# Kernel tuning notes

Measured on AMD Instinct MI355X. Metric: run time of the kernel, lower is better.

Reference implementation:

```python
import jax, jax.numpy as jnp
import numpy as np

B, GRID, WIDTH, NBLOCKS = 128, 32, 100, 50  # num_layers=100 -> 50 two-GEMM residual blocks


def _forward(inputs, W0, Wa, Wb, b1, b2, b3, b4, mult, Wout, bout):
    Bb, G = inputs.shape[0], inputs.shape[1]
    T = G // 2
    even = jnp.arange(0, G, 2)
    odd = even + 1
    idx = (even - 1) % G  # [(i-1) % G for even i]

    def patch(i1, i2):
        # gather axis1 then axis2 -> (B, T, T, 3, 3) flattened to (B*T*T, 9)
        return inputs[:, i1][:, :, i2].reshape(-1, 9)

    # order: right, left, up, down, center (matches tf.concat order)
    flat = jnp.concatenate([patch(odd, even), patch(idx, even), patch(even, odd),
                            patch(even, idx), patch(even, even)], axis=-1)  # (B*T*T, 45)

    x = jax.nn.relu(flat @ W0)  # (B*T*T, 100)

    def block(x, p):
        wa, wb, bb1, bb2, bb3, bb4, m = p
        x1 = (x + bb1) @ wa
        x1 = 2.0 * x1 + bb2          # x1 + bias_2 + x1
        x1 = jax.nn.relu(x1)
        x1 = 2.0 * x1 + bb3          # x1 + bias_3 + x1
        x1 = (x1 @ wb) * m
        x = jax.nn.relu(x + x1 + bb4)
        return x, None

    x, _ = jax.lax.scan(block, x, (Wa, Wb, b1, b2, b3, b4, mult))

    x = (x @ Wout + bout).reshape(Bb, T, T, 4)

    jp1 = (jnp.arange(T) + 1) % T
    jm1 = (jnp.arange(T) - 1) % T
    x0, x1c, x2, x3 = x[..., 0], x[..., 1], x[..., 2], x[..., 3]
    right_c = x0 / (x1c[:, jp1] + x0)
    left_c = x1c / (x1c + x0[:, jm1])
    up_c = x2 / (x2 + x3[:, :, jp1])
    down_c = x3 / (x2[:, :, jm1] + x3)

    # corner contributions from the original fine-grid stencils
    oo = inputs[:, odd][:, :, odd]    # odd-odd fine points (ru corner)
    oi = inputs[:, odd][:, :, idx]    # rd corner
    io = inputs[:, idx][:, :, odd]    # lu corner
    ii = inputs[:, idx][:, :, idx]    # ld corner
    ru = -(oo[..., 0, 0] + oo[..., 1, 0] * right_c + oo[..., 0, 1] * up_c) / oo[..., 1, 1]
    rd = -(oi[..., 0, 2] + oi[..., 1, 2] * right_c + oi[..., 0, 1] * down_c) / oi[..., 1, 1]
    lu = -(io[..., 2, 0] + io[..., 1, 0] * left_c + io[..., 2, 1] * up_c) / io[..., 1, 1]
    ld = -(ii[..., 2, 2] + ii[..., 1, 2] * left_c + ii[..., 2, 1] * down_c) / ii[..., 1, 1]

    ones = jnp.ones_like(down_c)
    first_row = jnp.stack([ld, left_c, lu], axis=-1)
    second_row = jnp.stack([down_c, ones, up_c], axis=-1)
    third_row = jnp.stack([rd, right_c, ru], axis=-1)
    out = jnp.stack([first_row, second_row, third_row], axis=0)  # (3, B, T, T, 3)
    return jnp.transpose(out, (1, 2, 3, 0, 4))  # (B, T, T, 3, 3)


def setup_inputs() -> dict:
    key = jax.random.key(0)
    ks = jax.random.split(key, 6)
    # positive stencil entries keep the corner divisions well-conditioned
    inputs = jax.random.uniform(ks[0], (B, GRID, GRID, 3, 3), jnp.float32) + 0.5
    W0 = jax.random.normal(ks[1], (45, WIDTH), jnp.float32) * np.float32(np.sqrt(2.0 / 45))
    Wa = jax.random.normal(ks[2], (NBLOCKS, WIDTH, WIDTH), jnp.float32) * np.float32(np.sqrt(2.0 / WIDTH))
    # original inits linear_{i+1} to zeros; small random keeps the baseline non-degenerate
    Wb = jax.random.normal(ks[3], (NBLOCKS, WIDTH, WIDTH), jnp.float32) * np.float32(0.01)
    b1 = jnp.zeros((NBLOCKS,), jnp.float32)
    b2 = jnp.zeros((NBLOCKS,), jnp.float32)
    b3 = jnp.zeros((NBLOCKS,), jnp.float32)
    b4 = jnp.zeros((NBLOCKS,), jnp.float32)
    mult = jnp.ones((NBLOCKS,), jnp.float32)
    Wout = jax.random.normal(ks[4], (WIDTH, 4), jnp.float32) * np.float32(0.05)
    bout = jnp.ones((4,), jnp.float32)  # keeps contribution denominators ~2 (stable)
    return {"inputs": inputs, "W0": W0, "Wa": Wa, "Wb": Wb, "b1": b1, "b2": b2,
            "b3": b3, "b4": b4, "mult": mult, "Wout": Wout, "bout": bout}


def reference(inputs, W0, Wa, Wb, b1, b2, b3, b4, mult, Wout, bout):
    return _forward(inputs, W0, Wa, Wb, b1, b2, b3, b4, mult, Wout, bout)
```

## Files before the change

kernel.cpp:

```cpp
#include <hip/hip_runtime.h>
#include <cstddef>

typedef _Float16 f16x8 __attribute__((ext_vector_type(8)));
typedef float f32x4 __attribute__((ext_vector_type(4)));

constexpr int BATCH = 128;
constexpr int T     = 16;
constexpr int ROWS  = BATCH * T * T;
constexpr int WID   = 100;
constexpr int NB    = 50;
constexpr int KP    = 128;
constexpr int NP    = 128;
constexpr int RPW   = 64;
constexpr int WCH   = 16384;

__global__ __launch_bounds__(256) void prep_kernel(
    const float* __restrict__ Wa, const float* __restrict__ Wb,
    _Float16* __restrict__ whi, _Float16* __restrict__ wlo,
    float* __restrict__ csA) {
  const int bid = blockIdx.x;
  const int bk = bid >> 1, m = bid & 1;
  const float* src = (m ? Wb : Wa) + (size_t)bk * (WID * WID);
  _Float16* dh = whi + (size_t)bid * WCH;
  _Float16* dl = wlo + (size_t)bid * WCH;
  for (int e = threadIdx.x; e < WCH; e += 256) {
    const int i   = e & 7;
    const int L   = (e >> 3) & 63;
    const int tau = (e >> 9) & 7;
    const int kap = e >> 12;
    const int k   = 32 * kap + (L >> 4) * 8 + i;
    const int col = 16 * tau + (L & 15);
    const float v = (k < WID && col < WID) ? src[k * WID + col] : 0.0f;
    const _Float16 hi = (_Float16)v;
    dh[e] = hi;
    dl[e] = (_Float16)(v - (float)hi);
  }
  if (!m) {
    for (int col = threadIdx.x; col < NP; col += 256) {
      float s = 0.0f;
      if (col < WID) {
        for (int k = 0; k < WID; ++k) s += src[k * WID + col];
      }
      csA[bk * NP + col] = s;
    }
  }
}

__global__ __launch_bounds__(256) void first_layer_kernel(
    const float* __restrict__ inp, const float* __restrict__ W0,
    float* __restrict__ x0) {
  __shared__ float w0s[45 * WID];
  for (int i = threadIdx.x; i < 45 * WID; i += 256) w0s[i] = W0[i];
  __syncthreads();

  const int rq  = threadIdx.x >> 2;
  const int cq  = threadIdx.x & 3;
  const int row = blockIdx.x * 64 + rq;
  const int b   = row >> 8;
  const int t1  = (row >> 4) & 15;
  const int t2  = row & 15;
  const int g1  = 2 * t1, g2 = 2 * t2;
  const int g1m = (g1 + 31) & 31, g2m = (g2 + 31) & 31;
  const float* base = inp + (size_t)b * (32 * 32 * 9);
  const float* p0 = base + ((g1 + 1) * 32 + g2) * 9;
  const float* p1 = base + (g1m * 32 + g2) * 9;
  const float* p2 = base + (g1 * 32 + (g2 + 1)) * 9;
  const float* p3 = base + (g1 * 32 + g2m) * 9;
  const float* p4 = base + (g1 * 32 + g2) * 9;

  float f[45];
#pragma unroll
  for (int qq = 0; qq < 9; ++qq) {
    f[qq]      = p0[qq];
    f[9 + qq]  = p1[qq];
    f[18 + qq] = p2[qq];
    f[27 + qq] = p3[qq];
    f[36 + qq] = p4[qq];
  }

  float acc[25];
#pragma unroll
  for (int j = 0; j < 25; ++j) acc[j] = 0.0f;
  const int j0 = cq * 25;
#pragma unroll
  for (int k = 0; k < 45; ++k) {
    const float fv = f[k];
#pragma unroll
    for (int j = 0; j < 25; ++j) acc[j] += fv * w0s[k * WID + j0 + j];
  }
  float* orow = x0 + (size_t)row * WID + j0;
#pragma unroll
  for (int j = 0; j < 25; ++j) orow[j] = fmaxf(acc[j], 0.0f);
}

__global__ __launch_bounds__(256, 2) void chain_kernel(
    float* __restrict__ x0,
    const _Float16* __restrict__ whi, const _Float16* __restrict__ wlo,
    const float* __restrict__ csA,
    const float* __restrict__ B1, const float* __restrict__ B2,
    const float* __restrict__ B3, const float* __restrict__ B4,
    const float* __restrict__ M) {
  __shared__ __align__(16) _Float16 xhs[RPW * KP];
  __shared__ __align__(16) _Float16 xls[RPW * KP];

  const int tid  = threadIdx.x;
  const int lane = tid & 63;
  const int uw   = __builtin_amdgcn_readfirstlane(tid >> 6);
  const int q    = lane >> 4;
  const int fr   = lane & 15;
  const int rbase = blockIdx.x * RPW;

  for (int i = tid; i < RPW * KP; i += 256) {
    const int row = i >> 7, k = i & 127;
    const float v = (k < WID) ? x0[(size_t)(rbase + row) * WID + k] : 0.0f;
    const _Float16 hi = (_Float16)v;
    const int a = row * KP + (k ^ ((row & 7) << 3));
    xhs[a] = hi;
    xls[a] = (_Float16)(v - (float)hi);
  }

  int colc[2];
#pragma unroll
  for (int c = 0; c < 2; ++c) colc[c] = 16 * (2 * uw + c) + fr;
  float xres[4][2][4];
#pragma unroll
  for (int rt = 0; rt < 4; ++rt)
#pragma unroll
    for (int c = 0; c < 2; ++c)
#pragma unroll
      for (int rg = 0; rg < 4; ++rg) {
        const int row = 16 * rt + 4 * q + rg;
        xres[rt][c][rg] = (colc[c] < WID)
            ? x0[(size_t)(rbase + row) * WID + colc[c]] : 0.0f;
      }
  __syncthreads();

  f32x4 acc[4][2];
  auto zero_acc = [&]() {
#pragma unroll
    for (int rt = 0; rt < 4; ++rt)
#pragma unroll
      for (int c = 0; c < 2; ++c) acc[rt][c] = (f32x4){0.f, 0.f, 0.f, 0.f};
  };

  auto kloop = [&](const _Float16* __restrict__ gh,
                   const _Float16* __restrict__ gl) {
    f16x8 bh[4][2], bl[4][2];
#pragma unroll
    for (int kap = 0; kap < 4; ++kap)
#pragma unroll
      for (int c = 0; c < 2; ++c) {
        const int off = (kap * 8 + 2 * uw + c) * 512 + lane * 8;
        bh[kap][c] = *(const f16x8*)&gh[off];
        bl[kap][c] = *(const f16x8*)&gl[off];
      }
#pragma unroll
    for (int kap = 0; kap < 4; ++kap) {
      f16x8 ah[4], al[4];
#pragma unroll
      for (int rt = 0; rt < 4; ++rt) {
        const int row = 16 * rt + fr;
        const int off = row * KP + ((32 * kap + 8 * q) ^ ((fr & 7) << 3));
        ah[rt] = *(const f16x8*)&xhs[off];
        al[rt] = *(const f16x8*)&xls[off];
      }
#pragma unroll
      for (int rt = 0; rt < 4; ++rt)
#pragma unroll
        for (int c = 0; c < 2; ++c) {
          acc[rt][c] = __builtin_amdgcn_mfma_f32_16x16x32_f16(
              ah[rt], bh[kap][c], acc[rt][c], 0, 0, 0);
          acc[rt][c] = __builtin_amdgcn_mfma_f32_16x16x32_f16(
              ah[rt], bl[kap][c], acc[rt][c], 0, 0, 0);
          acc[rt][c] = __builtin_amdgcn_mfma_f32_16x16x32_f16(
              al[rt], bh[kap][c], acc[rt][c], 0, 0, 0);
        }
    }
  };

  for (int bk = 0; bk < NB; ++bk) {
    zero_acc();
    kloop(whi + (size_t)(bk * 2) * WCH, wlo + (size_t)(bk * 2) * WCH);
    __syncthreads();
    {
      const float b1 = B1[bk], b2 = B2[bk], b3 = B3[bk];
      const float csv[2] = {csA[bk * NP + colc[0]], csA[bk * NP + colc[1]]};
#pragma unroll
      for (int rt = 0; rt < 4; ++rt)
#pragma unroll
        for (int c = 0; c < 2; ++c)
#pragma unroll
          for (int rg = 0; rg < 4; ++rg) {
            const int row = 16 * rt + 4 * q + rg;
            const float t = 2.0f * (acc[rt][c][rg] + b1 * csv[c]) + b2;
            const float v = 2.0f * fmaxf(t, 0.0f) + b3;
            const _Float16 hi = (_Float16)v;
            const int a = row * KP + (colc[c] ^ ((row & 7) << 3));
            xhs[a] = hi;
            xls[a] = (_Float16)(v - (float)hi);
          }
    }
    __syncthreads();

    zero_acc();
    kloop(whi + (size_t)(bk * 2 + 1) * WCH, wlo + (size_t)(bk * 2 + 1) * WCH);
    __syncthreads();
    {
      const float b4v = B4[bk], mm = M[bk];
#pragma unroll
      for (int rt = 0; rt < 4; ++rt)
#pragma unroll
        for (int c = 0; c < 2; ++c)
#pragma unroll
          for (int rg = 0; rg < 4; ++rg) {
            const int row = 16 * rt + 4 * q + rg;
            const float xn = fmaxf(xres[rt][c][rg] + acc[rt][c][rg] * mm + b4v, 0.0f);
            xres[rt][c][rg] = xn;
            const _Float16 hi = (_Float16)xn;
            const int a = row * KP + (colc[c] ^ ((row & 7) << 3));
            xhs[a] = hi;
            xls[a] = (_Float16)(xn - (float)hi);
          }
    }
    __syncthreads();
  }

#pragma unroll
  for (int rt = 0; rt < 4; ++rt)
#pragma unroll
    for (int c = 0; c < 2; ++c)
#pragma unroll
      for (int rg = 0; rg < 4; ++rg) {
        const int row = 16 * rt + 4 * q + rg;
        if (colc[c] < WID)
          x0[(size_t)(rbase + row) * WID + colc[c]] = xres[rt][c][rg];
      }
}

__global__ __launch_bounds__(256) void out_kernel(
    const float* __restrict__ inp, const float* __restrict__ x0,
    const float* __restrict__ Wout, const float* __restrict__ bout,
    float* __restrict__ out) {
  __shared__ float ys[256 * 4];
  __shared__ float wouts[WID * 4];
  __shared__ float bos[4];
  const int tid = threadIdx.x;
  const int b   = blockIdx.x;

  for (int i = tid; i < WID * 4; i += 256) wouts[i] = Wout[i];
  if (tid < 4) bos[tid] = bout[tid];
  __syncthreads();

  const int row = b * 256 + tid;
  const float* xr = x0 + (size_t)row * WID;
  float a0 = 0.f, a1 = 0.f, a2 = 0.f, a3 = 0.f;
#pragma unroll 4
  for (int k = 0; k < WID; ++k) {
    const float xv = xr[k];
    a0 += xv * wouts[k * 4 + 0];
    a1 += xv * wouts[k * 4 + 1];
    a2 += xv * wouts[k * 4 + 2];
    a3 += xv * wouts[k * 4 + 3];
  }
  ys[tid * 4 + 0] = a0 + bos[0];
  ys[tid * 4 + 1] = a1 + bos[1];
  ys[tid * 4 + 2] = a2 + bos[2];
  ys[tid * 4 + 3] = a3 + bos[3];
  __syncthreads();

  const int i = tid >> 4, j = tid & 15;
  const int ip1 = (i + 1) & 15, im1 = (i + 15) & 15;
  const int jp1 = (j + 1) & 15, jm1 = (j + 15) & 15;
  auto Y = [&](int a, int c, int comp) { return ys[(((a << 4) | c) << 2) + comp]; };
  const float y0 = Y(i, j, 0), y1 = Y(i, j, 1), y2 = Y(i, j, 2), y3 = Y(i, j, 3);
  const float right_c = y0 / (Y(ip1, j, 1) + y0);
  const float left_c  = y1 / (y1 + Y(im1, j, 0));
  const float up_c    = y2 / (y2 + Y(i, jp1, 3));
  const float down_c  = y3 / (Y(i, jm1, 2) + y3);

  const float* base = inp + (size_t)b * (32 * 32 * 9);
  const int g1 = 2 * i + 1, g1m = (2 * i + 31) & 31;
  const int g2 = 2 * j + 1, g2m = (2 * j + 31) & 31;
  const float* oo = base + (g1 * 32 + g2) * 9;
  const float* oi = base + (g1 * 32 + g2m) * 9;
  const float* io = base + (g1m * 32 + g2) * 9;
  const float* ii = base + (g1m * 32 + g2m) * 9;
  const float ru = -(oo[0] + oo[3] * right_c + oo[1] * up_c) / oo[4];
  const float rd = -(oi[2] + oi[5] * right_c + oi[1] * down_c) / oi[4];
  const float lu = -(io[6] + io[3] * left_c + io[7] * up_c) / io[4];
  const float ld = -(ii[8] + ii[5] * left_c + ii[7] * down_c) / ii[4];

  float* o = out + (size_t)row * 9;
  o[0] = ld;     o[1] = left_c;  o[2] = lu;
  o[3] = down_c; o[4] = 1.0f;    o[5] = up_c;
  o[6] = rd;     o[7] = right_c; o[8] = ru;
}

extern "C" void kernel_launch(void* const* d_in, const int* in_sizes, int n_in,
                              void* d_out, int out_size, void* d_ws, size_t ws_size,
                              hipStream_t stream) {
  const float* inp  = (const float*)d_in[0];
  const float* W0   = (const float*)d_in[1];
  const float* Wa   = (const float*)d_in[2];
  const float* Wb   = (const float*)d_in[3];
  const float* B1   = (const float*)d_in[4];
  const float* B2   = (const float*)d_in[5];
  const float* B3   = (const float*)d_in[6];
  const float* B4   = (const float*)d_in[7];
  const float* M    = (const float*)d_in[8];
  const float* Wout = (const float*)d_in[9];
  const float* bout = (const float*)d_in[10];
  float* out = (float*)d_out;

  float* ws       = (float*)d_ws;
  float* x0       = ws;
  _Float16* whi   = (_Float16*)(ws + 3276800);
  _Float16* wlo   = (_Float16*)(ws + 3276800 + 819200);
  float* csA      = ws + 3276800 + 819200 + 819200;

  hipLaunchKernelGGL(prep_kernel, dim3(100), dim3(256), 0, stream,
                     Wa, Wb, whi, wlo, csA);
  hipLaunchKernelGGL(first_layer_kernel, dim3(ROWS / 64), dim3(256), 0, stream,
                     inp, W0, x0);
  hipLaunchKernelGGL(chain_kernel, dim3(ROWS / RPW), dim3(256), 0, stream,
                     x0, whi, wlo, csA, B1, B2, B3, B4, M);
  hipLaunchKernelGGL(out_kernel, dim3(BATCH), dim3(256), 0, stream,
                     inp, x0, Wout, bout, out);
}
```

Before: 380.9 us.

## Halve rows per block and swap MFMA operands to compute transposed output tiles

```diff
diff --git a/kernel.cpp b/kernel.cpp
--- a/kernel.cpp
+++ b/kernel.cpp
@@ -2,6 +2,7 @@
 #include <cstddef>
 
 typedef _Float16 f16x8 __attribute__((ext_vector_type(8)));
+typedef _Float16 f16x4 __attribute__((ext_vector_type(4)));
 typedef float f32x4 __attribute__((ext_vector_type(4)));
 
 constexpr int BATCH = 128;
@@ -11,7 +12,7 @@
 constexpr int NB    = 50;
 constexpr int KP    = 128;
 constexpr int NP    = 128;
-constexpr int RPW   = 64;
+constexpr int RPW   = 32;
 constexpr int WCH   = 16384;
 
 __global__ __launch_bounds__(256) void prep_kernel(
@@ -119,61 +120,63 @@
     xls[a] = (_Float16)(v - (float)hi);
   }
 
-  int colc[2];
-#pragma unroll
-  for (int c = 0; c < 2; ++c) colc[c] = 16 * (2 * uw + c) + fr;
-  float xres[4][2][4];
-#pragma unroll
-  for (int rt = 0; rt < 4; ++rt)
-#pragma unroll
-    for (int c = 0; c < 2; ++c)
-#pragma unroll
-      for (int rg = 0; rg < 4; ++rg) {
-        const int row = 16 * rt + 4 * q + rg;
-        xres[rt][c][rg] = (colc[c] < WID)
-            ? x0[(size_t)(rbase + row) * WID + colc[c]] : 0.0f;
-      }
+  int j0c[2];
+#pragma unroll
+  for (int c = 0; c < 2; ++c) j0c[c] = 16 * (2 * uw + c) + 4 * q;
+
+  f32x4 xres[2][2];
+#pragma unroll
+  for (int nt = 0; nt < 2; ++nt)
+#pragma unroll
+    for (int c = 0; c < 2; ++c) {
+      const int row = 16 * nt + fr;
+      if (j0c[c] < WID) {
+        xres[nt][c] = *(const f32x4*)&x0[(size_t)(rbase + row) * WID + j0c[c]];
+      } else {
+        xres[nt][c] = (f32x4){0.f, 0.f, 0.f, 0.f};
+      }
+    }
   __syncthreads();
 
-  f32x4 acc[4][2];
+  f32x4 acc[2][2];
   auto zero_acc = [&]() {
 #pragma unroll
-    for (int rt = 0; rt < 4; ++rt)
-#pragma unroll
-      for (int c = 0; c < 2; ++c) acc[rt][c] = (f32x4){0.f, 0.f, 0.f, 0.f};
+    for (int nt = 0; nt < 2; ++nt)
+#pragma unroll
+      for (int c = 0; c < 2; ++c) acc[nt][c] = (f32x4){0.f, 0.f, 0.f, 0.f};
   };
 
   auto kloop = [&](const _Float16* __restrict__ gh,
                    const _Float16* __restrict__ gl) {
-    f16x8 bh[4][2], bl[4][2];
+    f16x8 wh[4][2], wl[4][2];
 #pragma unroll
     for (int kap = 0; kap < 4; ++kap)
 #pragma unroll
       for (int c = 0; c < 2; ++c) {
         const int off = (kap * 8 + 2 * uw + c) * 512 + lane * 8;
-        bh[kap][c] = *(const f16x8*)&gh[off];
-        bl[kap][c] = *(const f16x8*)&gl[off];
+        wh[kap][c] = *(const f16x8*)&gh[off];
+        wl[kap][c] = *(const f16x8*)&gl[off];
       }
 #pragma unroll
     for (int kap = 0; kap < 4; ++kap) {
-      f16x8 ah[4], al[4];
-#pragma unroll
-      for (int rt = 0; rt < 4; ++rt) {
-        const int row = 16 * rt + fr;
+      f16x8 xh_[2], xl_[2];
+#pragma unroll
+      for (int nt = 0; nt < 2; ++nt) {
+        const int row = 16 * nt + fr;
         const int off = row * KP + ((32 * kap + 8 * q) ^ ((fr & 7) << 3));
-        ah[rt] = *(const f16x8*)&xhs[off];
-        al[rt] = *(const f16x8*)&xls[off];
-      }
-#pragma unroll
-      for (int rt = 0; rt < 4; ++rt)
+        xh_[nt] = *(const f16x8*)&xhs[off];
+        xl_[nt] = *(const f16x8*)&xls[off];
+      }
+#pragma unroll
+      for (int nt = 0; nt < 2; ++nt)
 #pragma unroll
         for (int c = 0; c < 2; ++c) {
-          acc[rt][c] = __builtin_amdgcn_mfma_f32_16x16x32_f16(
-              ah[rt], bh[kap][c], acc[rt][c], 0, 0, 0);
-          acc[rt][c] = __builtin_amdgcn_mfma_f32_16x16x32_f16(
-              ah[rt], bl[kap][c], acc[rt][c], 0, 0, 0);
-          acc[rt][c] = __builtin_amdgcn_mfma_f32_16x16x32_f16(
-              al[rt], bh[kap][c], acc[rt][c], 0, 0, 0);
+          acc[nt][c] = __builtin_amdgcn_mfma_f32_16x16x32_f16(
+              wh[kap][c], xh_[nt], acc[nt][c], 0, 0, 0);
+          acc[nt][c] = __builtin_amdgcn_mfma_f32_16x16x32_f16(
+              wl[kap][c], xh_[nt], acc[nt][c], 0, 0, 0);
+          acc[nt][c] = __builtin_amdgcn_mfma_f32_16x16x32_f16(
+              wh[kap][c], xl_[nt], acc[nt][c], 0, 0, 0);
         }
     }
   };
@@ -184,21 +187,28 @@
     __syncthreads();
     {
       const float b1 = B1[bk], b2 = B2[bk], b3 = B3[bk];
-      const float csv[2] = {csA[bk * NP + colc[0]], csA[bk * NP + colc[1]]};
-#pragma unroll
-      for (int rt = 0; rt < 4; ++rt)
-#pragma unroll
-        for (int c = 0; c < 2; ++c)
-#pragma unroll
-          for (int rg = 0; rg < 4; ++rg) {
-            const int row = 16 * rt + 4 * q + rg;
-            const float t = 2.0f * (acc[rt][c][rg] + b1 * csv[c]) + b2;
-            const float v = 2.0f * fmaxf(t, 0.0f) + b3;
-            const _Float16 hi = (_Float16)v;
-            const int a = row * KP + (colc[c] ^ ((row & 7) << 3));
-            xhs[a] = hi;
-            xls[a] = (_Float16)(v - (float)hi);
+#pragma unroll
+      for (int c = 0; c < 2; ++c) {
+        if (j0c[c] < WID) {
+          const f32x4 cs = *(const f32x4*)&csA[bk * NP + j0c[c]];
+#pragma unroll
+          for (int nt = 0; nt < 2; ++nt) {
+            const int row = 16 * nt + fr;
+            f16x4 hv, lv;
+#pragma unroll
+            for (int r = 0; r < 4; ++r) {
+              const float t = 2.0f * (acc[nt][c][r] + b1 * cs[r]) + b2;
+              const float v = 2.0f * fmaxf(t, 0.0f) + b3;
+              const _Float16 hi = (_Float16)v;
+              hv[r] = hi;
+              lv[r] = (_Float16)(v - (float)hi);
+            }
+            const int a = row * KP + (j0c[c] ^ ((row & 7) << 3));
+            *(f16x4*)&xhs[a] = hv;
+            *(f16x4*)&xls[a] = lv;
           }
+        }
+      }
     }
     __syncthreads();
 
@@ -208,33 +218,38 @@
     {
       const float b4v = B4[bk], mm = M[bk];
 #pragma unroll
-      for (int rt = 0; rt < 4; ++rt)
-#pragma unroll
-        for (int c = 0; c < 2; ++c)
-#pragma unroll
-          for (int rg = 0; rg < 4; ++rg) {
-            const int row = 16 * rt + 4 * q + rg;
-            const float xn = fmaxf(xres[rt][c][rg] + acc[rt][c][rg] * mm + b4v, 0.0f);
-            xres[rt][c][rg] = xn;
-            const _Float16 hi = (_Float16)xn;
-            const int a = row * KP + (colc[c] ^ ((row & 7) << 3));
-            xhs[a] = hi;
-            xls[a] = (_Float16)(xn - (float)hi);
+      for (int c = 0; c < 2; ++c) {
+        if (j0c[c] < WID) {
+#pragma unroll
+          for (int nt = 0; nt < 2; ++nt) {
+            const int row = 16 * nt + fr;
+            f16x4 hv, lv;
+#pragma unroll
+            for (int r = 0; r < 4; ++r) {
+              const float xn = fmaxf(xres[nt][c][r] + acc[nt][c][r] * mm + b4v, 0.0f);
+              xres[nt][c][r] = xn;
+              const _Float16 hi = (_Float16)xn;
+              hv[r] = hi;
+              lv[r] = (_Float16)(xn - (float)hi);
+            }
+            const int a = row * KP + (j0c[c] ^ ((row & 7) << 3));
+            *(f16x4*)&xhs[a] = hv;
+            *(f16x4*)&xls[a] = lv;
           }
+        }
+      }
     }
     __syncthreads();
   }
 
 #pragma unroll
-  for (int rt = 0; rt < 4; ++rt)
-#pragma unroll
-    for (int c = 0; c < 2; ++c)
-#pragma unroll
-      for (int rg = 0; rg < 4; ++rg) {
-        const int row = 16 * rt + 4 * q + rg;
-        if (colc[c] < WID)
-          x0[(size_t)(rbase + row) * WID + colc[c]] = xres[rt][c][rg];
-      }
+  for (int nt = 0; nt < 2; ++nt)
+#pragma unroll
+    for (int c = 0; c < 2; ++c) {
+      const int row = 16 * nt + fr;
+      if (j0c[c] < WID)
+        *(f32x4*)&x0[(size_t)(rbase + row) * WID + j0c[c]] = xres[nt][c];
+    }
 }
 
 __global__ __launch_bounds__(256) void out_kernel(
```

Result: slower. 503.8 us (+32.3%).
